# Optimization experiments

Measured on AMD Instinct MI355X. Metric: run time of the kernel, lower is better.

Reference implementation:

```python
import jax, jax.numpy as jnp
import numpy as np

INPUT_DIM = 32
HID_DIM = 64
TTCN_DIM = HID_DIM - 1  # 63
N, LX = 128, 512


def setup_inputs() -> dict:
    key = jax.random.key(0)
    ks = jax.random.split(key, 10)
    X_int = jax.random.normal(ks[0], (N, LX, INPUT_DIM), dtype=jnp.float32)
    mask_X = jax.random.randint(ks[1], (N, LX, 1), 0, 2).astype(jnp.float32)
    s1 = 1.0 / np.sqrt(INPUT_DIM)
    s2 = 1.0 / np.sqrt(TTCN_DIM)
    W1 = jax.random.uniform(ks[2], (INPUT_DIM, TTCN_DIM), jnp.float32, -s1, s1)
    b1 = jax.random.uniform(ks[3], (TTCN_DIM,), jnp.float32, -s1, s1)
    W2 = jax.random.uniform(ks[4], (TTCN_DIM, TTCN_DIM), jnp.float32, -s2, s2)
    b2 = jax.random.uniform(ks[5], (TTCN_DIM,), jnp.float32, -s2, s2)
    W3 = jax.random.uniform(ks[6], (TTCN_DIM, INPUT_DIM * TTCN_DIM), jnp.float32, -s2, s2)
    b3 = jax.random.uniform(ks[7], (INPUT_DIM * TTCN_DIM,), jnp.float32, -s2, s2)
    T_bias = jax.random.normal(ks[8], (1, TTCN_DIM), dtype=jnp.float32)
    return {"X_int": X_int, "mask_X": mask_X, "W1": W1, "b1": b1,
            "W2": W2, "b2": b2, "W3": W3, "b3": b3, "T_bias": T_bias}


def reference(X_int, mask_X, W1, b1, W2, b2, W3, b3, T_bias):
    n, lx, d = X_int.shape
    k = TTCN_DIM
    # 3-layer MLP filter generator: (N, Lx, D*K)
    h = jax.nn.relu(X_int @ W1 + b1)
    h = jax.nn.relu(h @ W2 + b2)
    filt = h @ W3 + b3
    # masked softmax over the time axis Lx
    filt = filt * mask_X + (1.0 - mask_X) * (-1e8)
    filt = jax.nn.softmax(filt, axis=1)  # softmax over Lx
    filt = filt.reshape(n, lx, k, d)     # (N, Lx, K, D)
    # attention-weighted pooling: sum over Lx and D
    out = jnp.einsum('nld,nlkd->nk', X_int, filt)
    return jax.nn.relu(out + T_bias)
```

## Files before the change

### kernel.cpp

```cpp
#include <hip/hip_runtime.h>
#include <hip/hip_bf16.h>


#define N_   128
#define LX_  512
#define D_   32
#define K_   63
#define C_   2016
#define LOG2E 1.44269504088896f

typedef __bf16 bf16x8 __attribute__((ext_vector_type(8)));
typedef float floatx4 __attribute__((ext_vector_type(4)));
typedef float floatx2 __attribute__((ext_vector_type(2)));

static __device__ __forceinline__ floatx4 mfma16(bf16x8 a, bf16x8 b, floatx4 c) {
  return __builtin_amdgcn_mfma_f32_16x16x32_bf16(a, b, c, 0, 0, 0);
}

#define HC_OFF   0u
#define XT_OFF   (8u * 1024u * 1024u)
#define W3FR_OFF (16u * 1024u * 1024u)
#define W1FR_OFF (W3FR_OFF + 258048u)
#define W2FR_OFF (W1FR_OFF + 4096u)
#define B1_OFF   (W2FR_OFF + 8192u)
#define POS_OFF  (B1_OFF + 256u)
#define CNT_OFF  (POS_OFF + 262144u)

__global__ __launch_bounds__(256) void kern_prep(
    const float* __restrict__ Mk,
    const float* __restrict__ W1, const float* __restrict__ b1,
    const float* __restrict__ W2, const float* __restrict__ b2,
    const float* __restrict__ W3, const float* __restrict__ b3,
    __bf16* __restrict__ W3fr, __bf16* __restrict__ W1fr,
    __bf16* __restrict__ W2fr, float* __restrict__ b1pad,
    int* __restrict__ pos, int* __restrict__ cnt,
    __bf16* __restrict__ Hc, float* __restrict__ Xt) {
  const int n = blockIdx.x, tid = threadIdx.x;
  __shared__ int s_cnt;

  if (tid < 64) {
    const int lane = tid;
    int running = 0;
#pragma unroll
    for (int c = 0; c < 8; ++c) {
      const int l = c * 64 + lane;
      const float mkv = Mk[n * LX_ + l];
      const unsigned long long b = __ballot(mkv > 0.5f);
      const int mypos = running + __popcll(b & ((1ull << lane) - 1ull));
      pos[n * LX_ + l] = (mkv > 0.5f) ? mypos : -1;
      running += __popcll(b);
    }
    if (lane == 0) { cnt[n] = running; s_cnt = running; }
  }
  __syncthreads();

  const int c0 = s_cnt, c1 = (c0 + 63) & ~63;
  const float4 z = {0.f, 0.f, 0.f, 0.f};
  for (int idx = tid; idx < (c1 - c0) * 40; idx += 256) {
    const int row = c0 + idx / 40, q = idx % 40;
    if (q < 8) {
      *(float4*)(Hc + ((size_t)(n * 512 + row)) * 64 + q * 8) = z;
    } else {
      const int d = q - 8;
      Xt[((size_t)(n * 32 + (row >> 4)) * 32 + d) * 16 + (row & 15)] = 0.f;
    }
  }

  for (int g = n * 256 + tid; g < 129024 + 2048 + 4096 + 64; g += N_ * 256) {
    if (g < 129024) {
      const int j = g & 7, quad = (g >> 3) & 3, l16 = (g >> 5) & 15, h = (g >> 9) & 1;
      const int rest = g >> 10, i = rest % 6, tile = rest / 6;
      const int c = tile * 96 + i * 16 + l16;
      const int t = h * 32 + quad * 8 + j;
      W3fr[g] = (__bf16)(((t < K_) ? W3[(size_t)t * C_ + c] : b3[c]) * LOG2E);
    } else if (g < 129024 + 2048) {
      const int g2 = g - 129024;
      const int j = g2 & 7, quad = (g2 >> 3) & 3, l16 = (g2 >> 5) & 15, i = g2 >> 9;
      const int ch = i * 16 + l16, t = quad * 8 + j;
      W1fr[g2] = (__bf16)((ch < K_) ? W1[t * K_ + ch] : 0.f);
    } else if (g < 129024 + 2048 + 4096) {
      const int g2 = g - 129024 - 2048;
      const int j = g2 & 7, quad = (g2 >> 3) & 3, l16 = (g2 >> 5) & 15, h = (g2 >> 9) & 1;
      const int i = g2 >> 10;
      const int ch = i * 16 + l16, t = h * 32 + quad * 8 + j;
      float v;
      if (t < K_) v = (ch < K_) ? W2[t * K_ + ch] : 0.f;
      else        v = (ch < K_) ? b2[ch] : 1.f;
      W2fr[g2] = (__bf16)v;
    } else {
      const int g2 = g - 129024 - 2048 - 4096;
      b1pad[g2] = (g2 < K_) ? b1[g2] : 0.f;
    }
  }
}

__global__ __launch_bounds__(256) void kern_mlp(
    const float* __restrict__ X, const __bf16* __restrict__ W1fr,
    const __bf16* __restrict__ W2fr, const float* __restrict__ b1pad,
    const int* __restrict__ pos, __bf16* __restrict__ Hc,
    float* __restrict__ Xt) {
  __shared__ float h1s[4][16][68];
  const int tid = threadIdx.x;
  const int w = tid >> 6, lane = tid & 63, quad = lane >> 4, l16 = lane & 15;

  bf16x8 b1f[4], b2f[4][2];
  float b1v[4];
#pragma unroll
  for (int i = 0; i < 4; ++i) {
    b1f[i]    = *(const bf16x8*)(W1fr + ((i * 16 + l16) * 4 + quad) * 8);
    b2f[i][0] = *(const bf16x8*)(W2fr + (((i * 2 + 0) * 16 + l16) * 4 + quad) * 8);
    b2f[i][1] = *(const bf16x8*)(W2fr + (((i * 2 + 1) * 16 + l16) * 4 + quad) * 8);
    b1v[i] = b1pad[i * 16 + l16];
  }

  const int tok0 = blockIdx.x * 64 + w * 16;
  const int n = tok0 >> 9;
  const float* xp = X + (size_t)(tok0 + l16) * D_ + quad * 8;
  const float4 xa = *(const float4*)xp;
  const float4 xb = *(const float4*)(xp + 4);
  bf16x8 a1;
  a1[0]=(__bf16)xa.x; a1[1]=(__bf16)xa.y; a1[2]=(__bf16)xa.z; a1[3]=(__bf16)xa.w;
  a1[4]=(__bf16)xb.x; a1[5]=(__bf16)xb.y; a1[6]=(__bf16)xb.z; a1[7]=(__bf16)xb.w;

  const int px = pos[tok0 + l16];
  int pr[4];
#pragma unroll
  for (int r = 0; r < 4; ++r) pr[r] = pos[tok0 + quad * 4 + r];

  if (px >= 0) {
    float* xtp = Xt + ((size_t)(n * 32 + (px >> 4)) * 32 + quad * 8) * 16 + (px & 15);
    const float vals[8] = {xa.x, xa.y, xa.z, xa.w, xb.x, xb.y, xb.z, xb.w};
#pragma unroll
    for (int j = 0; j < 8; ++j) xtp[j * 16] = vals[j];
  }

#pragma unroll
  for (int i = 0; i < 4; ++i) {
    floatx4 acc = {0.f, 0.f, 0.f, 0.f};
    acc = mfma16(a1, b1f[i], acc);
#pragma unroll
    for (int r = 0; r < 4; ++r) {
      float v = fmaxf(acc[r] + b1v[i], 0.f);
      if (i == 3 && l16 == 15) v = 1.f;
      h1s[w][quad * 4 + r][i * 16 + l16] = v;
    }
  }

  const float* hrow = &h1s[w][l16][0];
  const float4 p0 = *(const float4*)(hrow + quad * 8);
  const float4 p1 = *(const float4*)(hrow + quad * 8 + 4);
  const float4 p2 = *(const float4*)(hrow + 32 + quad * 8);
  const float4 p3 = *(const float4*)(hrow + 32 + quad * 8 + 4);
  bf16x8 a20, a21;
  a20[0]=(__bf16)p0.x; a20[1]=(__bf16)p0.y; a20[2]=(__bf16)p0.z; a20[3]=(__bf16)p0.w;
  a20[4]=(__bf16)p1.x; a20[5]=(__bf16)p1.y; a20[6]=(__bf16)p1.z; a20[7]=(__bf16)p1.w;
  a21[0]=(__bf16)p2.x; a21[1]=(__bf16)p2.y; a21[2]=(__bf16)p2.z; a21[3]=(__bf16)p2.w;
  a21[4]=(__bf16)p3.x; a21[5]=(__bf16)p3.y; a21[6]=(__bf16)p3.z; a21[7]=(__bf16)p3.w;

#pragma unroll
  for (int i = 0; i < 4; ++i) {
    floatx4 acc = {0.f, 0.f, 0.f, 0.f};
    acc = mfma16(a20, b2f[i][0], acc);
    acc = mfma16(a21, b2f[i][1], acc);
#pragma unroll
    for (int r = 0; r < 4; ++r) {
      if (pr[r] >= 0)
        Hc[((size_t)(n * 512 + pr[r])) * 64 + i * 16 + l16] =
            (__bf16)fmaxf(acc[r], 0.f);
    }
  }
}

__global__ __launch_bounds__(256) void kern_att(
    const __bf16* __restrict__ Hc, const float* __restrict__ Xt,
    const __bf16* __restrict__ W3fr, const int* __restrict__ cnt,
    const float* __restrict__ Tb, float* __restrict__ out) {
  __shared__ float redS[4][96], redO[4][96];
  __shared__ float rbuf[96];

  const int bid = blockIdx.x;
  const int idx = bid >> 3;
  const int n = (bid & 7) * 16 + idx / 21;
  const int bt = idx % 21;
  const int tid = threadIdx.x;
  const int w = tid >> 6, lane = tid & 63, quad = lane >> 4, l16 = lane & 15;

  bf16x8 bf[6][2];
#pragma unroll
  for (int i = 0; i < 6; ++i) {
    bf[i][0] = *(const bf16x8*)(W3fr + ((((bt * 6 + i) * 2 + 0) * 16 + l16) * 4 + quad) * 8);
    bf[i][1] = *(const bf16x8*)(W3fr + ((((bt * 6 + i) * 2 + 1) * 16 + l16) * 4 + quad) * 8);
  }

  const int cntn = cnt[n];
  const int nch = (cntn + 15) >> 4;
  const __bf16* Hb = Hc + ((size_t)n << 9) * 64 + (size_t)l16 * 64 + quad * 8;
  const float*  Xb = Xt + ((size_t)n * 32) * 512 + l16 * 16 + quad * 4;

  floatx2 s2[3] = {{0.f, 0.f}, {0.f, 0.f}, {0.f, 0.f}};
  float o[6] = {0, 0, 0, 0, 0, 0};

  int c = w;
  bf16x8 a0 = *(const bf16x8*)(Hb + (size_t)c * 1024);
  bf16x8 a1 = *(const bf16x8*)(Hb + (size_t)c * 1024 + 32);
  float4 xl4 = *(const float4*)(Xb + c * 512);
  float4 xh4 = *(const float4*)(Xb + c * 512 + 256);

#pragma unroll 1
  while (c < nch) {
    const int cn = c + 4;
    bf16x8 na0, na1;
    float4 nxl, nxh;
    if (cn < nch) {
      na0 = *(const bf16x8*)(Hb + (size_t)cn * 1024);
      na1 = *(const bf16x8*)(Hb + (size_t)cn * 1024 + 32);
      nxl = *(const float4*)(Xb + cn * 512);
      nxh = *(const float4*)(Xb + cn * 512 + 256);
    }

#pragma unroll
    for (int t = 0; t < 3; ++t) {
      floatx4 accE = {0.f, 0.f, 0.f, 0.f};
      floatx4 accO = {0.f, 0.f, 0.f, 0.f};
      accE = mfma16(a0, bf[2 * t][0], accE);
      accE = mfma16(a1, bf[2 * t][1], accE);
      accO = mfma16(a0, bf[2 * t + 1][0], accO);
      accO = mfma16(a1, bf[2 * t + 1][1], accO);
#pragma unroll
      for (int r = 0; r < 4; ++r) {
        floatx2 e2;
        e2.x = __builtin_amdgcn_exp2f(accE[r]);
        e2.y = __builtin_amdgcn_exp2f(accO[r]);
        s2[t] += e2;
        o[2 * t]     = fmaf(e2.x, xl4[r], o[2 * t]);
        o[2 * t + 1] = fmaf(e2.y, xh4[r], o[2 * t + 1]);
      }
    }

    c = cn;
    a0 = na0; a1 = na1; xl4 = nxl; xh4 = nxh;
  }

#pragma unroll
  for (int t = 0; t < 3; ++t) {
    s2[t].x += __shfl_xor(s2[t].x, 16); s2[t].x += __shfl_xor(s2[t].x, 32);
    s2[t].y += __shfl_xor(s2[t].y, 16); s2[t].y += __shfl_xor(s2[t].y, 32);
  }
#pragma unroll
  for (int i = 0; i < 6; ++i) {
    o[i] += __shfl_xor(o[i], 16);
    o[i] += __shfl_xor(o[i], 32);
  }
  if (quad == 0) {
#pragma unroll
    for (int t = 0; t < 3; ++t) {
      redS[w][(2 * t) * 16 + l16]     = s2[t].x;
      redS[w][(2 * t + 1) * 16 + l16] = s2[t].y;
    }
#pragma unroll
    for (int i = 0; i < 6; ++i) redO[w][i * 16 + l16] = o[i];
  }
  __syncthreads();
  if (tid < 96) {
    const float pad = (float)(nch * 16 - cntn);
    const float S = redS[0][tid] + redS[1][tid] + redS[2][tid] + redS[3][tid] - pad;
    const float O = redO[0][tid] + redO[1][tid] + redO[2][tid] + redO[3][tid];
    rbuf[tid] = O / S;
  }
  __syncthreads();
  if (tid < 3) {
    float acc = 0.f;
#pragma unroll
    for (int dd = 0; dd < 32; ++dd) acc += rbuf[tid * 32 + dd];
    const int k = bt * 3 + tid;
    out[n * K_ + k] = fmaxf(acc + Tb[k], 0.f);
  }
}

extern "C" void kernel_launch(void* const* d_in, const int* in_sizes, int n_in,
                              void* d_out, int out_size, void* d_ws, size_t ws_size,
                              hipStream_t stream) {
  const float* X  = (const float*)d_in[0];
  const float* Mk = (const float*)d_in[1];
  const float* W1 = (const float*)d_in[2];
  const float* b1 = (const float*)d_in[3];
  const float* W2 = (const float*)d_in[4];
  const float* b2 = (const float*)d_in[5];
  const float* W3 = (const float*)d_in[6];
  const float* b3 = (const float*)d_in[7];
  const float* Tb = (const float*)d_in[8];
  float* out = (float*)d_out;

  char* ws = (char*)d_ws;
  __bf16* Hc    = (__bf16*)(ws + HC_OFF);
  float*  Xt    = (float*)(ws + XT_OFF);
  __bf16* W3fr  = (__bf16*)(ws + W3FR_OFF);
  __bf16* W1fr  = (__bf16*)(ws + W1FR_OFF);
  __bf16* W2fr  = (__bf16*)(ws + W2FR_OFF);
  float*  b1pad = (float*)(ws + B1_OFF);
  int*    pos   = (int*)(ws + POS_OFF);
  int*    cnt   = (int*)(ws + CNT_OFF);

  kern_prep<<<N_, 256, 0, stream>>>(Mk, W1, b1, W2, b2, W3, b3,
                                    W3fr, W1fr, W2fr, b1pad, pos, cnt, Hc, Xt);
  kern_mlp<<<N_ * LX_ / 64, 256, 0, stream>>>(X, W1fr, W2fr, b1pad, pos, Hc, Xt);
  kern_att<<<N_ * 21, 256, 0, stream>>>(Hc, Xt, W3fr, cnt, Tb, out);
}
```

Measured before the change: 112.4 us.

## Fold prep kernel into MLP kernel and recompute mask compaction per block

Removes the separate prep launch. W3 fragment packing moves into 128 extra blocks of the MLP kernel. Each MLP block rebuilds the W1/W2 fragments in shared memory and recomputes compacted positions from the mask with a wave-level prefix scan, and the attention kernel recounts valid tokens from the mask. Padding rows are no longer zeroed and are instead masked in the last chunk of the attention loop. This cuts one launch and its serial dependency, at the cost of redundant per-block weight conversion and mask scans.

```diff
diff --git a/kernel.cpp b/kernel.cpp
--- a/kernel.cpp
+++ b/kernel.cpp
@@ -20,112 +20,101 @@
 #define HC_OFF   0u
 #define XT_OFF   (8u * 1024u * 1024u)
 #define W3FR_OFF (16u * 1024u * 1024u)
-#define W1FR_OFF (W3FR_OFF + 258048u)
-#define W2FR_OFF (W1FR_OFF + 4096u)
-#define B1_OFF   (W2FR_OFF + 8192u)
-#define POS_OFF  (B1_OFF + 256u)
-#define CNT_OFF  (POS_OFF + 262144u)
-
-__global__ __launch_bounds__(256) void kern_prep(
-    const float* __restrict__ Mk,
+
+__global__ __launch_bounds__(256) void kern_mlp(
+    const float* __restrict__ X, const float* __restrict__ Mk,
     const float* __restrict__ W1, const float* __restrict__ b1,
     const float* __restrict__ W2, const float* __restrict__ b2,
     const float* __restrict__ W3, const float* __restrict__ b3,
-    __bf16* __restrict__ W3fr, __bf16* __restrict__ W1fr,
-    __bf16* __restrict__ W2fr, float* __restrict__ b1pad,
-    int* __restrict__ pos, int* __restrict__ cnt,
-    __bf16* __restrict__ Hc, float* __restrict__ Xt) {
-  const int n = blockIdx.x, tid = threadIdx.x;
-  __shared__ int s_cnt;
-
-  if (tid < 64) {
-    const int lane = tid;
-    int running = 0;
-#pragma unroll
-    for (int c = 0; c < 8; ++c) {
-      const int l = c * 64 + lane;
-      const float mkv = Mk[n * LX_ + l];
-      const unsigned long long b = __ballot(mkv > 0.5f);
-      const int mypos = running + __popcll(b & ((1ull << lane) - 1ull));
-      pos[n * LX_ + l] = (mkv > 0.5f) ? mypos : -1;
-      running += __popcll(b);
-    }
-    if (lane == 0) { cnt[n] = running; s_cnt = running; }
-  }
-  __syncthreads();
-
-  const int c0 = s_cnt, c1 = (c0 + 63) & ~63;
-  const float4 z = {0.f, 0.f, 0.f, 0.f};
-  for (int idx = tid; idx < (c1 - c0) * 40; idx += 256) {
-    const int row = c0 + idx / 40, q = idx % 40;
-    if (q < 8) {
-      *(float4*)(Hc + ((size_t)(n * 512 + row)) * 64 + q * 8) = z;
-    } else {
-      const int d = q - 8;
-      Xt[((size_t)(n * 32 + (row >> 4)) * 32 + d) * 16 + (row & 15)] = 0.f;
-    }
-  }
-
-  for (int g = n * 256 + tid; g < 129024 + 2048 + 4096 + 64; g += N_ * 256) {
-    if (g < 129024) {
-      const int j = g & 7, quad = (g >> 3) & 3, l16 = (g >> 5) & 15, h = (g >> 9) & 1;
+    __bf16* __restrict__ W3fr, __bf16* __restrict__ Hc,
+    float* __restrict__ Xt) {
+  const int tid = threadIdx.x;
+
+  if (blockIdx.x < 128) {
+    for (int g = blockIdx.x * 256 + tid; g < 129024; g += 128 * 256) {
+      const int j = g & 7, quad = (g >> 3) & 3, l16v = (g >> 5) & 15, h = (g >> 9) & 1;
       const int rest = g >> 10, i = rest % 6, tile = rest / 6;
-      const int c = tile * 96 + i * 16 + l16;
+      const int cch = tile * 96 + i * 16 + l16v;
       const int t = h * 32 + quad * 8 + j;
-      W3fr[g] = (__bf16)(((t < K_) ? W3[(size_t)t * C_ + c] : b3[c]) * LOG2E);
-    } else if (g < 129024 + 2048) {
-      const int g2 = g - 129024;
-      const int j = g2 & 7, quad = (g2 >> 3) & 3, l16 = (g2 >> 5) & 15, i = g2 >> 9;
-      const int ch = i * 16 + l16, t = quad * 8 + j;
-      W1fr[g2] = (__bf16)((ch < K_) ? W1[t * K_ + ch] : 0.f);
-    } else if (g < 129024 + 2048 + 4096) {
-      const int g2 = g - 129024 - 2048;
-      const int j = g2 & 7, quad = (g2 >> 3) & 3, l16 = (g2 >> 5) & 15, h = (g2 >> 9) & 1;
-      const int i = g2 >> 10;
-      const int ch = i * 16 + l16, t = h * 32 + quad * 8 + j;
-      float v;
-      if (t < K_) v = (ch < K_) ? W2[t * K_ + ch] : 0.f;
-      else        v = (ch < K_) ? b2[ch] : 1.f;
-      W2fr[g2] = (__bf16)v;
-    } else {
-      const int g2 = g - 129024 - 2048 - 4096;
-      b1pad[g2] = (g2 < K_) ? b1[g2] : 0.f;
-    }
-  }
-}
-
-__global__ __launch_bounds__(256) void kern_mlp(
-    const float* __restrict__ X, const __bf16* __restrict__ W1fr,
-    const __bf16* __restrict__ W2fr, const float* __restrict__ b1pad,
-    const int* __restrict__ pos, __bf16* __restrict__ Hc,
-    float* __restrict__ Xt) {
+      W3fr[g] = (__bf16)(((t < K_) ? W3[(size_t)t * C_ + cch] : b3[cch]) * LOG2E);
+    }
+    return;
+  }
+
   __shared__ float h1s[4][16][68];
-  const int tid = threadIdx.x;
+  __shared__ __align__(16) __bf16 W1s[2048];
+  __shared__ __align__(16) __bf16 W2s[4096];
+  __shared__ float b1s[64];
+
   const int w = tid >> 6, lane = tid & 63, quad = lane >> 4, l16 = lane & 15;
-
-  bf16x8 b1f[4], b2f[4][2];
-  float b1v[4];
-#pragma unroll
-  for (int i = 0; i < 4; ++i) {
-    b1f[i]    = *(const bf16x8*)(W1fr + ((i * 16 + l16) * 4 + quad) * 8);
-    b2f[i][0] = *(const bf16x8*)(W2fr + (((i * 2 + 0) * 16 + l16) * 4 + quad) * 8);
-    b2f[i][1] = *(const bf16x8*)(W2fr + (((i * 2 + 1) * 16 + l16) * 4 + quad) * 8);
-    b1v[i] = b1pad[i * 16 + l16];
-  }
-
-  const int tok0 = blockIdx.x * 64 + w * 16;
+  const int bid = blockIdx.x - 128;
+  const int tok0 = bid * 64 + w * 16;
   const int n = tok0 >> 9;
+  const int tile0 = tok0 & 511;
+
   const float* xp = X + (size_t)(tok0 + l16) * D_ + quad * 8;
   const float4 xa = *(const float4*)xp;
   const float4 xb = *(const float4*)(xp + 4);
+  const float4 mq0 = *(const float4*)(Mk + n * 512 + lane * 8);
+  const float4 mq1 = *(const float4*)(Mk + n * 512 + lane * 8 + 4);
+
+  for (int g = tid; g < 2048; g += 256) {
+    const int j = g & 7, qd = (g >> 3) & 3, lv = (g >> 5) & 15, i = g >> 9;
+    const int ch = i * 16 + lv, t = qd * 8 + j;
+    W1s[g] = (__bf16)((ch < K_) ? W1[t * K_ + ch] : 0.f);
+  }
+  for (int g = tid; g < 4096; g += 256) {
+    const int j = g & 7, qd = (g >> 3) & 3, lv = (g >> 5) & 15, h = (g >> 9) & 1;
+    const int i = g >> 10;
+    const int ch = i * 16 + lv, t = h * 32 + qd * 8 + j;
+    float v;
+    if (t < K_) v = (ch < K_) ? W2[t * K_ + ch] : 0.f;
+    else        v = (ch < K_) ? b2[ch] : 1.f;
+    W2s[g] = (__bf16)v;
+  }
+  if (tid < 64) b1s[tid] = (tid < K_) ? b1[tid] : 0.f;
+  __syncthreads();
+
+  unsigned mbits = (mq0.x > 0.5f ? 1u : 0u) | (mq0.y > 0.5f ? 2u : 0u) |
+                   (mq0.z > 0.5f ? 4u : 0u) | (mq0.w > 0.5f ? 8u : 0u) |
+                   (mq1.x > 0.5f ? 16u : 0u) | (mq1.y > 0.5f ? 32u : 0u) |
+                   (mq1.z > 0.5f ? 64u : 0u) | (mq1.w > 0.5f ? 128u : 0u);
+  const int pc = __popc(mbits);
+  int scan = pc;
+#pragma unroll
+  for (int d = 1; d < 64; d <<= 1) {
+    const int t = __shfl_up(scan, d);
+    if (lane >= d) scan += t;
+  }
+  const int excl = scan - pc;
+
+  const int jA = (tile0 >> 3) + (l16 >> 3), bA = l16 & 7;
+  const unsigned mA = (unsigned)__shfl((int)mbits, jA);
+  const int eA = __shfl(excl, jA);
+  const int px = ((mA >> bA) & 1u) ? (eA + __popc(mA & ((1u << bA) - 1u))) : -1;
+  int pr[4];
+#pragma unroll
+  for (int r = 0; r < 4; ++r) {
+    const int lr = quad * 4 + r;
+    const int jR = (tile0 >> 3) + (lr >> 3), bR = lr & 7;
+    const unsigned mR = (unsigned)__shfl((int)mbits, jR);
+    const int eR = __shfl(excl, jR);
+    pr[r] = ((mR >> bR) & 1u) ? (eR + __popc(mR & ((1u << bR) - 1u))) : -1;
+  }
+
+  bf16x8 b1f[4], b2f[4][2];
+  float b1v[4];
+#pragma unroll
+  for (int i = 0; i < 4; ++i) {
+    b1f[i]    = *(const bf16x8*)(&W1s[((i * 16 + l16) * 4 + quad) * 8]);
+    b2f[i][0] = *(const bf16x8*)(&W2s[(((i * 2 + 0) * 16 + l16) * 4 + quad) * 8]);
+    b2f[i][1] = *(const bf16x8*)(&W2s[(((i * 2 + 1) * 16 + l16) * 4 + quad) * 8]);
+    b1v[i] = b1s[i * 16 + l16];
+  }
+
   bf16x8 a1;
   a1[0]=(__bf16)xa.x; a1[1]=(__bf16)xa.y; a1[2]=(__bf16)xa.z; a1[3]=(__bf16)xa.w;
   a1[4]=(__bf16)xb.x; a1[5]=(__bf16)xb.y; a1[6]=(__bf16)xb.z; a1[7]=(__bf16)xb.w;
-
-  const int px = pos[tok0 + l16];
-  int pr[4];
-#pragma unroll
-  for (int r = 0; r < 4; ++r) pr[r] = pos[tok0 + quad * 4 + r];
 
   if (px >= 0) {
     float* xtp = Xt + ((size_t)(n * 32 + (px >> 4)) * 32 + quad * 8) * 16 + (px & 15);
@@ -173,7 +162,7 @@
 
 __global__ __launch_bounds__(256) void kern_att(
     const __bf16* __restrict__ Hc, const float* __restrict__ Xt,
-    const __bf16* __restrict__ W3fr, const int* __restrict__ cnt,
+    const __bf16* __restrict__ W3fr, const float* __restrict__ Mk,
     const float* __restrict__ Tb, float* __restrict__ out) {
   __shared__ float redS[4][96], redO[4][96];
   __shared__ float rbuf[96];
@@ -185,6 +174,9 @@
   const int tid = threadIdx.x;
   const int w = tid >> 6, lane = tid & 63, quad = lane >> 4, l16 = lane & 15;
 
+  const float4 mq0 = *(const float4*)(Mk + n * 512 + lane * 8);
+  const float4 mq1 = *(const float4*)(Mk + n * 512 + lane * 8 + 4);
+
   bf16x8 bf[6][2];
 #pragma unroll
   for (int i = 0; i < 6; ++i) {
@@ -192,7 +184,12 @@
     bf[i][1] = *(const bf16x8*)(W3fr + ((((bt * 6 + i) * 2 + 1) * 16 + l16) * 4 + quad) * 8);
   }
 
-  const int cntn = cnt[n];
+  int pc = (mq0.x > 0.5f) + (mq0.y > 0.5f) + (mq0.z > 0.5f) + (mq0.w > 0.5f) +
+           (mq1.x > 0.5f) + (mq1.y > 0.5f) + (mq1.z > 0.5f) + (mq1.w > 0.5f);
+#pragma unroll
+  for (int d = 1; d < 64; d <<= 1) pc += __shfl_xor(pc, d);
+  const int cntn = pc;
+
   const int nch = (cntn + 15) >> 4;
   const __bf16* Hb = Hc + ((size_t)n << 9) * 64 + (size_t)l16 * 64 + quad * 8;
   const float*  Xb = Xt + ((size_t)n * 32) * 512 + l16 * 16 + quad * 4;
@@ -200,22 +197,34 @@
   floatx2 s2[3] = {{0.f, 0.f}, {0.f, 0.f}, {0.f, 0.f}};
   float o[6] = {0, 0, 0, 0, 0, 0};
 
+  bf16x8 zb;
+#pragma unroll
+  for (int j = 0; j < 8; ++j) zb[j] = (__bf16)0.f;
+
   int c = w;
   bf16x8 a0 = *(const bf16x8*)(Hb + (size_t)c * 1024);
   bf16x8 a1 = *(const bf16x8*)(Hb + (size_t)c * 1024 + 32);
-  float4 xl4 = *(const float4*)(Xb + c * 512);
-  float4 xh4 = *(const float4*)(Xb + c * 512 + 256);
+  floatx4 xl4 = *(const floatx4*)(Xb + c * 512);
+  floatx4 xh4 = *(const floatx4*)(Xb + c * 512 + 256);
 
 #pragma unroll 1
   while (c < nch) {
     const int cn = c + 4;
     bf16x8 na0, na1;
-    float4 nxl, nxh;
+    floatx4 nxl, nxh;
     if (cn < nch) {
       na0 = *(const bf16x8*)(Hb + (size_t)cn * 1024);
       na1 = *(const bf16x8*)(Hb + (size_t)cn * 1024 + 32);
-      nxl = *(const float4*)(Xb + cn * 512);
-      nxh = *(const float4*)(Xb + cn * 512 + 256);
+      nxl = *(const floatx4*)(Xb + cn * 512);
+      nxh = *(const floatx4*)(Xb + cn * 512 + 256);
+    }
+
+    if (c == nch - 1) {
+      const int rem = cntn - (c << 4);
+      if (l16 >= rem) { a0 = zb; a1 = zb; }
+#pragma unroll
+      for (int r = 0; r < 4; ++r)
+        if (quad * 4 + r >= rem) { xl4[r] = 0.f; xh4[r] = 0.f; }
     }
 
 #pragma unroll
@@ -292,17 +301,11 @@
   float* out = (float*)d_out;
 
   char* ws = (char*)d_ws;
-  __bf16* Hc    = (__bf16*)(ws + HC_OFF);
-  float*  Xt    = (float*)(ws + XT_OFF);
-  __bf16* W3fr  = (__bf16*)(ws + W3FR_OFF);
-  __bf16* W1fr  = (__bf16*)(ws + W1FR_OFF);
-  __bf16* W2fr  = (__bf16*)(ws + W2FR_OFF);
-  float*  b1pad = (float*)(ws + B1_OFF);
-  int*    pos   = (int*)(ws + POS_OFF);
-  int*    cnt   = (int*)(ws + CNT_OFF);
-
-  kern_prep<<<N_, 256, 0, stream>>>(Mk, W1, b1, W2, b2, W3, b3,
-                                    W3fr, W1fr, W2fr, b1pad, pos, cnt, Hc, Xt);
-  kern_mlp<<<N_ * LX_ / 64, 256, 0, stream>>>(X, W1fr, W2fr, b1pad, pos, Hc, Xt);
-  kern_att<<<N_ * 21, 256, 0, stream>>>(Hc, Xt, W3fr, cnt, Tb, out);
+  __bf16* Hc   = (__bf16*)(ws + HC_OFF);
+  float*  Xt   = (float*)(ws + XT_OFF);
+  __bf16* W3fr = (__bf16*)(ws + W3FR_OFF);
+
+  kern_mlp<<<128 + N_ * LX_ / 64, 256, 0, stream>>>(X, Mk, W1, b1, W2, b2, W3, b3,
+                                                    W3fr, Hc, Xt);
+  kern_att<<<N_ * 21, 256, 0, stream>>>(Hc, Xt, W3fr, Mk, Tb, out);
 }
```

New measurement: 115.2 us. 1.03x slower.
